# Performance work log

Measured on AMD Instinct MI355X. Metric: run time of the kernel, lower is better.

Reference implementation:

```python
import jax, jax.numpy as jnp
import numpy as np

B, D = 4096, 128
TEMPERATURE = 0.2

def setup_inputs() -> dict:
    key = jax.random.key(0)
    k1, k2 = jax.random.split(key)
    z1 = jax.random.normal(k1, (B, D), dtype=jnp.float32)
    z2 = jax.random.normal(k2, (B, D), dtype=jnp.float32)
    return {"z1": z1, "z2": z2}

def reference(z1, z2):
    # single-process path: global batch == local batch
    gb = z1.shape[0]
    z = jnp.concatenate([z1, z2], axis=0)              # [2B, D]
    sim = jnp.matmul(z, z.T) / TEMPERATURE             # [2B, 2B]
    n = 2 * gb
    diag = jnp.eye(n, dtype=bool)
    sim = jnp.where(diag, jnp.finfo(sim.dtype).min, sim)
    targets = jnp.concatenate([jnp.arange(gb, n), jnp.arange(0, gb)])
    logp = jax.nn.log_softmax(sim, axis=-1)            # [2B, 2B]
    loss_all = -logp[jnp.arange(n), targets]           # [2B]
    # rank 0, world_size 1 -> idx_keep covers all rows
    return loss_all.mean()
```

## Files before the change

kernel.cpp:

```cpp
#include <hip/hip_runtime.h>
#include <stdint.h>

typedef unsigned short u16;
typedef unsigned int u32;

#define NTOT 8192
#define BH   4096
#define DD   128
#define COLSPLIT 16
#define COLS_PER_SPLIT (NTOT / COLSPLIT)
#define TILE_COLS 64
#define TILES_PER_SPLIT (COLS_PER_SPLIT / TILE_COLS)
#define ROWS_PER_BLOCK 128
#define ROWS_PER_WAVE 32
#define TILE_U16 (TILE_COLS * DD)
#define NEG_INF (-3.0e38f)
#define SCALE_IN 2.68579144f
#define LN2F 0.6931471805599453f

typedef __bf16 bf16x8 __attribute__((ext_vector_type(8)));
typedef float  f32x4  __attribute__((ext_vector_type(4)));

__device__ __forceinline__ u16 f2bf(float f) {
  u32 u = __float_as_uint(f);
  return (u16)((u + 0x7fffu + ((u >> 16) & 1u)) >> 16);
}

__device__ __forceinline__ float fexp2(float x) {
#if __has_builtin(__builtin_amdgcn_exp2f)
  return __builtin_amdgcn_exp2f(x);
#else
  float r; asm("v_exp_f32 %0, %1" : "=v"(r) : "v"(x)); return r;
#endif
}

__global__ __launch_bounds__(256) void ntx_convert(
    const float* __restrict__ z1, const float* __restrict__ z2,
    u16* __restrict__ zb, float* __restrict__ out) {
  if (blockIdx.x == 0 && threadIdx.x == 0) out[0] = 0.f;
  const int i = (blockIdx.x * 256 + threadIdx.x) * 4;
  const int half = BH * DD;
  float4 v = (i < half) ? *reinterpret_cast<const float4*>(z1 + i)
                        : *reinterpret_cast<const float4*>(z2 + (i - half));
  u32 lo = (u32)f2bf(v.x * SCALE_IN) | ((u32)f2bf(v.y * SCALE_IN) << 16);
  u32 hi = (u32)f2bf(v.z * SCALE_IN) | ((u32)f2bf(v.w * SCALE_IN) << 16);
  uint2 o; o.x = lo; o.y = hi;
  *reinterpret_cast<uint2*>(zb + i) = o;
}

__global__ __launch_bounds__(256, 4) void ntx_main(
    const u16* __restrict__ zb,
    float* __restrict__ m_part, float* __restrict__ l_part,
    float* __restrict__ st_part) {
  __shared__ u16 lds_tile[2][TILE_U16];

  const int tid  = threadIdx.x;
  const int wave = tid >> 6;
  const int lane = tid & 63;
  const int l15  = lane & 15;
  const int q    = lane >> 4;

  const int rwave = blockIdx.x * ROWS_PER_BLOCK + wave * ROWS_PER_WAVE;
  const int split = blockIdx.y;
  const int col0  = split * COLS_PER_SPLIT;

#define STAGE_TILE(buf, ct0_)                                                  \
  {                                                                            \
    _Pragma("unroll")                                                          \
    for (int j = 0; j < 4; ++j) {                                              \
      const int j4   = wave * 4 + j;                                           \
      const int col  = j4 * 4 + (lane >> 4);                                   \
      const int slot = (lane & 15) ^ (col & 7);                                \
      const u16* srcp = zb + ((ct0_) + col) * DD + slot * 8;                   \
      u16* dstp = &lds_tile[(buf)][j4 * 512 + lane * 8];                       \
      __builtin_amdgcn_global_load_lds(                                        \
          (const __attribute__((address_space(1))) u32*)srcp,                  \
          (__attribute__((address_space(3))) u32*)dstp, 16, 0, 0);             \
    }                                                                          \
  }

  bf16x8 afrag[2][4];
#pragma unroll
  for (int rt = 0; rt < 2; ++rt)
#pragma unroll
    for (int kk = 0; kk < 4; ++kk) {
      const int r = rwave + rt * 16 + l15;
      afrag[rt][kk] = *reinterpret_cast<const bf16x8*>(zb + r * DD + kk * 32 + q * 8);
    }

  float m_run[2][4], l_run[2][4], stv[2][4];
#pragma unroll
  for (int rt = 0; rt < 2; ++rt)
#pragma unroll
    for (int r = 0; r < 4; ++r) { m_run[rt][r] = NEG_INF; l_run[rt][r] = 0.f; stv[rt][r] = NEG_INF; }

  STAGE_TILE(0, col0)
  __syncthreads();

  for (int t = 0; t < TILES_PER_SPLIT; ++t) {
    const int ct0 = col0 + t * TILE_COLS;
    const int cur = t & 1;

    if (t + 1 < TILES_PER_SPLIT) STAGE_TILE(cur ^ 1, ct0 + TILE_COLS)

    const u16* bb = &lds_tile[cur][0];

    f32x4 acc[2][4];
#pragma unroll
    for (int rt = 0; rt < 2; ++rt)
#pragma unroll
      for (int cs = 0; cs < 4; ++cs) acc[rt][cs] = (f32x4){0.f, 0.f, 0.f, 0.f};

#pragma unroll
    for (int cs = 0; cs < 4; ++cs) {
      const int col = cs * 16 + l15;
      const int xr  = col & 7;
      bf16x8 bfrag[4];
#pragma unroll
      for (int kk = 0; kk < 4; ++kk)
        bfrag[kk] = *reinterpret_cast<const bf16x8*>(
            bb + col * DD + (((kk * 4 + q) ^ xr) * 8));
#pragma unroll
      for (int rt = 0; rt < 2; ++rt)
#pragma unroll
        for (int kk = 0; kk < 4; ++kk)
          acc[rt][cs] = __builtin_amdgcn_mfma_f32_16x16x32_bf16(
              afrag[rt][kk], bfrag[kk], acc[rt][cs], 0, 0, 0);
    }

    const bool has_diag = (rwave >= ct0) && (rwave < ct0 + TILE_COLS);
    const int  trow     = rwave ^ BH;
    const bool has_tgt  = (trow >= ct0) && (trow < ct0 + TILE_COLS);
    if (has_diag || has_tgt) {
#pragma unroll
      for (int rt = 0; rt < 2; ++rt)
#pragma unroll
        for (int r = 0; r < 4; ++r) {
          const int grow = rwave + rt * 16 + q * 4 + r;
#pragma unroll
          for (int cs = 0; cs < 4; ++cs) {
            const int gcol = ct0 + cs * 16 + l15;
            float v = acc[rt][cs][r];
            if (gcol == (grow ^ BH)) stv[rt][r] = fmaxf(stv[rt][r], v);
            if (gcol == grow) acc[rt][cs][r] = NEG_INF;
          }
        }
    }

#pragma unroll
    for (int rt = 0; rt < 2; ++rt)
#pragma unroll
      for (int r = 0; r < 4; ++r) {
        float mx = fmaxf(fmaxf(acc[rt][0][r], acc[rt][1][r]),
                         fmaxf(acc[rt][2][r], acc[rt][3][r]));
        const float mnew = fmaxf(m_run[rt][r], mx);
        float s = 0.f;
#pragma unroll
        for (int cs = 0; cs < 4; ++cs) s += fexp2(acc[rt][cs][r] - mnew);
        l_run[rt][r] = l_run[rt][r] * fexp2(m_run[rt][r] - mnew) + s;
        m_run[rt][r] = mnew;
      }

    __syncthreads();
  }

#pragma unroll
  for (int rt = 0; rt < 2; ++rt)
#pragma unroll
    for (int r = 0; r < 4; ++r) {
      float m = m_run[rt][r], l = l_run[rt][r];
#pragma unroll
      for (int off = 1; off < 16; off <<= 1) {
        const float mo = __shfl_xor(m, off, 64);
        const float lo = __shfl_xor(l, off, 64);
        const float mn = fmaxf(m, mo);
        l = l * fexp2(m - mn) + lo * fexp2(mo - mn);
        m = mn;
      }
      float sv = stv[rt][r];
#pragma unroll
      for (int off = 1; off < 16; off <<= 1) sv = fmaxf(sv, __shfl_xor(sv, off, 64));
      if (l15 == 0) {
        const int grow = rwave + rt * 16 + q * 4 + r;
        m_part[split * NTOT + grow] = m;
        l_part[split * NTOT + grow] = l;
        const int tcol = grow ^ BH;
        if (tcol >= col0 && tcol < col0 + COLS_PER_SPLIT) st_part[grow] = sv;
      }
    }
#undef STAGE_TILE
}

__global__ __launch_bounds__(256) void ntx_finish(
    const float* __restrict__ m_part, const float* __restrict__ l_part,
    const float* __restrict__ st_part, float* __restrict__ out) {
  const int row = blockIdx.x * 256 + threadIdx.x;
  float m = NEG_INF;
#pragma unroll
  for (int s = 0; s < COLSPLIT; ++s) m = fmaxf(m, m_part[s * NTOT + row]);
  float l = 0.f;
#pragma unroll
  for (int s = 0; s < COLSPLIT; ++s) l += l_part[s * NTOT + row] * fexp2(m_part[s * NTOT + row] - m);
  float loss = LN2F * (m + __log2f(l) - st_part[row]);

#pragma unroll
  for (int off = 32; off >= 1; off >>= 1) loss += __shfl_xor(loss, off, 64);
  __shared__ float wsum[4];
  if ((threadIdx.x & 63) == 0) wsum[threadIdx.x >> 6] = loss;
  __syncthreads();
  if (threadIdx.x == 0) {
    float s = wsum[0] + wsum[1] + wsum[2] + wsum[3];
    atomicAdd(out, s * (1.0f / NTOT));
  }
}

extern "C" void kernel_launch(void* const* d_in, const int* in_sizes, int n_in,
                              void* d_out, int out_size, void* d_ws, size_t ws_size,
                              hipStream_t stream) {
  const float* z1 = (const float*)d_in[0];
  const float* z2 = (const float*)d_in[1];
  float* out = (float*)d_out;

  char* ws = (char*)d_ws;
  u16*   zb      = (u16*)ws;
  float* m_part  = (float*)(ws + (size_t)NTOT * DD * 2);
  float* l_part  = m_part + COLSPLIT * NTOT;
  float* st_part = l_part + COLSPLIT * NTOT;

  ntx_convert<<<dim3((NTOT * DD) / (256 * 4)), dim3(256), 0, stream>>>(z1, z2, zb, out);
  ntx_main<<<dim3(NTOT / ROWS_PER_BLOCK, COLSPLIT), dim3(256), 0, stream>>>(
      zb, m_part, l_part, st_part);
  ntx_finish<<<dim3(NTOT / 256), dim3(256), 0, stream>>>(m_part, l_part, st_part, out);
}
```

Measured before the change: 90.07 us.

## Software-pipeline MFMA and softmax across tiles with dual accumulators

```diff
diff --git a/kernel.cpp b/kernel.cpp
--- a/kernel.cpp
+++ b/kernel.cpp
@@ -7,7 +7,7 @@
 #define NTOT 8192
 #define BH   4096
 #define DD   128
-#define COLSPLIT 16
+#define COLSPLIT 8
 #define COLS_PER_SPLIT (NTOT / COLSPLIT)
 #define TILE_COLS 64
 #define TILES_PER_SPLIT (COLS_PER_SPLIT / TILE_COLS)
@@ -48,7 +48,7 @@
   *reinterpret_cast<uint2*>(zb + i) = o;
 }
 
-__global__ __launch_bounds__(256, 4) void ntx_main(
+__global__ __launch_bounds__(256, 2) void ntx_main(
     const u16* __restrict__ zb,
     float* __restrict__ m_part, float* __restrict__ l_part,
     float* __restrict__ st_part) {
@@ -79,6 +79,69 @@
     }                                                                          \
   }
 
+#define MFMA_TILE(ACC, BUF)                                                    \
+  {                                                                            \
+    _Pragma("unroll")                                                          \
+    for (int rt = 0; rt < 2; ++rt)                                             \
+      _Pragma("unroll")                                                        \
+      for (int cs = 0; cs < 4; ++cs) ACC[rt][cs] = (f32x4){0.f,0.f,0.f,0.f};   \
+    const u16* bb = &lds_tile[(BUF)][0];                                       \
+    _Pragma("unroll")                                                          \
+    for (int cs = 0; cs < 4; ++cs) {                                           \
+      const int col = cs * 16 + l15;                                           \
+      const int xr  = col & 7;                       \
+      bf16x8 bfrag[4];                                                         \
+      _Pragma("unroll")                                                        \
+      for (int kk = 0; kk < 4; ++kk)                                           \
+        bfrag[kk] = *reinterpret_cast<const bf16x8*>(                          \
+            bb + col * DD + (((kk * 4 + q) ^ xr) * 8));                        \
+      _Pragma("unroll")                                                        \
+      for (int rt = 0; rt < 2; ++rt)                                           \
+        _Pragma("unroll")                                                      \
+        for (int kk = 0; kk < 4; ++kk)                                         \
+          ACC[rt][cs] = __builtin_amdgcn_mfma_f32_16x16x32_bf16(               \
+              afrag[rt][kk], bfrag[kk], ACC[rt][cs], 0, 0, 0);                 \
+    }                                                                          \
+  }
+
+#define SOFTMAX_TILE(ACC, CT0)                                                 \
+  {                                                                            \
+    const int ct0_ = (CT0);                                                    \
+    const bool has_diag = (rwave >= ct0_) && (rwave < ct0_ + TILE_COLS);       \
+    const int  trow     = rwave ^ BH;                                          \
+    const bool has_tgt  = (trow >= ct0_) && (trow < ct0_ + TILE_COLS);         \
+    if (has_diag || has_tgt) {                                                 \
+      _Pragma("unroll")                                                        \
+      for (int rt = 0; rt < 2; ++rt)                                           \
+        _Pragma("unroll")                                                      \
+        for (int r = 0; r < 4; ++r) {                                          \
+          const int grow = rwave + rt * 16 + q * 4 + r;                        \
+          _Pragma("unroll")                                                    \
+          for (int cs = 0; cs < 4; ++cs) {                                     \
+            const int gcol = ct0_ + cs * 16 + l15;                             \
+            float v = ACC[rt][cs][r];                                          \
+            if (gcol == (grow ^ BH)) stv[rt][r] = fmaxf(stv[rt][r], v);        \
+            if (gcol == grow) ACC[rt][cs][r] = NEG_INF;                        \
+          }                                                                    \
+        }                                                                      \
+    }                                                                          \
+    _Pragma("unroll")                                                          \
+    for (int rt = 0; rt < 2; ++rt)                                             \
+      _Pragma("unroll")                                                        \
+      for (int r = 0; r < 4; ++r) {                                            \
+        float mx = fmaxf(fmaxf(ACC[rt][0][r], ACC[rt][1][r]),                  \
+                         fmaxf(ACC[rt][2][r], ACC[rt][3][r]));                 \
+        const float mnew = fmaxf(m_run[rt][r], mx);                            \
+        float s = 0.f;                                                         \
+        _Pragma("unroll")                                                      \
+        for (int cs = 0; cs < 4; ++cs) s += fexp2(ACC[rt][cs][r] - mnew);      \
+        l_run[rt][r] = l_run[rt][r] * fexp2(m_run[rt][r] - mnew) + s;          \
+        m_run[rt][r] = mnew;                                                   \
+      }                                                                        \
+  }
+
+  STAGE_TILE(0, col0)
+
   bf16x8 afrag[2][4];
 #pragma unroll
   for (int rt = 0; rt < 2; ++rt)
@@ -94,75 +157,29 @@
 #pragma unroll
     for (int r = 0; r < 4; ++r) { m_run[rt][r] = NEG_INF; l_run[rt][r] = 0.f; stv[rt][r] = NEG_INF; }
 
-  STAGE_TILE(0, col0)
   __syncthreads();
 
-  for (int t = 0; t < TILES_PER_SPLIT; ++t) {
-    const int ct0 = col0 + t * TILE_COLS;
-    const int cur = t & 1;
-
-    if (t + 1 < TILES_PER_SPLIT) STAGE_TILE(cur ^ 1, ct0 + TILE_COLS)
-
-    const u16* bb = &lds_tile[cur][0];
-
-    f32x4 acc[2][4];
-#pragma unroll
-    for (int rt = 0; rt < 2; ++rt)
-#pragma unroll
-      for (int cs = 0; cs < 4; ++cs) acc[rt][cs] = (f32x4){0.f, 0.f, 0.f, 0.f};
-
-#pragma unroll
-    for (int cs = 0; cs < 4; ++cs) {
-      const int col = cs * 16 + l15;
-      const int xr  = col & 7;
-      bf16x8 bfrag[4];
-#pragma unroll
-      for (int kk = 0; kk < 4; ++kk)
-        bfrag[kk] = *reinterpret_cast<const bf16x8*>(
-            bb + col * DD + (((kk * 4 + q) ^ xr) * 8));
-#pragma unroll
-      for (int rt = 0; rt < 2; ++rt)
-#pragma unroll
-        for (int kk = 0; kk < 4; ++kk)
-          acc[rt][cs] = __builtin_amdgcn_mfma_f32_16x16x32_bf16(
-              afrag[rt][kk], bfrag[kk], acc[rt][cs], 0, 0, 0);
-    }
-
-    const bool has_diag = (rwave >= ct0) && (rwave < ct0 + TILE_COLS);
-    const int  trow     = rwave ^ BH;
-    const bool has_tgt  = (trow >= ct0) && (trow < ct0 + TILE_COLS);
-    if (has_diag || has_tgt) {
-#pragma unroll
-      for (int rt = 0; rt < 2; ++rt)
-#pragma unroll
-        for (int r = 0; r < 4; ++r) {
-          const int grow = rwave + rt * 16 + q * 4 + r;
-#pragma unroll
-          for (int cs = 0; cs < 4; ++cs) {
-            const int gcol = ct0 + cs * 16 + l15;
-            float v = acc[rt][cs][r];
-            if (gcol == (grow ^ BH)) stv[rt][r] = fmaxf(stv[rt][r], v);
-            if (gcol == grow) acc[rt][cs][r] = NEG_INF;
-          }
-        }
-    }
-
-#pragma unroll
-    for (int rt = 0; rt < 2; ++rt)
-#pragma unroll
-      for (int r = 0; r < 4; ++r) {
-        float mx = fmaxf(fmaxf(acc[rt][0][r], acc[rt][1][r]),
-                         fmaxf(acc[rt][2][r], acc[rt][3][r]));
-        const float mnew = fmaxf(m_run[rt][r], mx);
-        float s = 0.f;
-#pragma unroll
-        for (int cs = 0; cs < 4; ++cs) s += fexp2(acc[rt][cs][r] - mnew);
-        l_run[rt][r] = l_run[rt][r] * fexp2(m_run[rt][r] - mnew) + s;
-        m_run[rt][r] = mnew;
-      }
-
+  f32x4 accA[2][4], accB[2][4];
+
+  STAGE_TILE(1, col0 + TILE_COLS)
+  MFMA_TILE(accA, 0)
+  __syncthreads();
+
+  for (int tp = 1; tp + 1 < TILES_PER_SPLIT; tp += 2) {
+    STAGE_TILE(0, col0 + (tp + 1) * TILE_COLS)
+    MFMA_TILE(accB, 1)
+    SOFTMAX_TILE(accA, col0 + (tp - 1) * TILE_COLS)
     __syncthreads();
-  }
+
+    STAGE_TILE(1, col0 + (tp + 2) * TILE_COLS)
+    MFMA_TILE(accA, 0)
+    SOFTMAX_TILE(accB, col0 + tp * TILE_COLS)
+    __syncthreads();
+  }
+
+  MFMA_TILE(accB, 1)
+  SOFTMAX_TILE(accA, col0 + (TILES_PER_SPLIT - 2) * TILE_COLS)
+  SOFTMAX_TILE(accB, col0 + (TILES_PER_SPLIT - 1) * TILE_COLS)
 
 #pragma unroll
   for (int rt = 0; rt < 2; ++rt)
@@ -189,6 +206,8 @@
       }
     }
 #undef STAGE_TILE
+#undef MFMA_TILE
+#undef SOFTMAX_TILE
 }
 
 __global__ __launch_bounds__(256) void ntx_finish(
```

New measurement: 88.34 us. About the same (-1.9%).
